# Kernel optimization log

Hardware: AMD Instinct MI355X
Metric: run time of the kernel (lower is better)

The kernel has to match this reference:

```python
import jax, jax.numpy as jnp
import numpy as np

NUM_FEATURE = 50


def setup_inputs() -> dict:
    key = jax.random.key(0)
    k1, k2 = jax.random.split(key)
    query = jax.random.normal(k1, (512, NUM_FEATURE), dtype=jnp.float32)
    doc = jax.random.normal(k2, (512, 256, NUM_FEATURE), dtype=jnp.float32)
    # nn.Linear(150, 1, bias=False) with weight filled with 1
    W = jnp.ones((3 * NUM_FEATURE,), dtype=jnp.float32)
    return {"query": query, "doc": doc, "W": W}


def reference(query, doc, W):
    # Split the single 150-dim linear weight into the three trilinear parts:
    # score(x, y) = w1.sen_x + w2.q_y + w3.(sen_x * q_y)
    w1, w2, w3 = W[:NUM_FEATURE], W[NUM_FEATURE:2 * NUM_FEATURE], W[2 * NUM_FEATURE:]
    q_term = query @ w2                      # [Lq]
    qw3 = query * w3                         # [Lq, d]

    def per_sentence(sen):                   # sen: [Ls, d]
        sXY = (sen @ w1)[:, None] + q_term[None, :] + sen @ qw3.T   # [Ls, Lq]
        sD2Q = jax.nn.softmax(sXY, axis=0)   # softmax over sentence tokens
        sQ2D = jax.nn.softmax(sXY, axis=1)   # softmax over query tokens
        aD2Q = sD2Q @ query                  # [Ls, d]
        aQ2D = sD2Q @ (sQ2D.T @ sen)         # (sD2Q @ sQ2D.T) @ sen, cheaper order
        return jnp.concatenate([sen, aD2Q, sen * aD2Q, sen * aQ2D], axis=1)  # [Ls, 4d]

    return jax.vmap(per_sentence)(doc)       # [n_sen, Ls, 4d]
```

## Files before the change

### kernel.cpp

```cpp
#include <hip/hip_runtime.h>
#include <math.h>

typedef __bf16 bf16_t;
typedef bf16_t bf16x2 __attribute__((ext_vector_type(2)));
typedef bf16_t bf16x4 __attribute__((ext_vector_type(4)));
typedef bf16_t bf16x8 __attribute__((ext_vector_type(8)));
typedef float f32x4 __attribute__((ext_vector_type(4)));

#define MFMA16(a,b,c) __builtin_amdgcn_mfma_f32_16x16x32_bf16((a),(b),(c),0,0,0)

#define ND 256
#define NQ 512
#define NF 50
#define L2E 1.44269504f
#define SHIFT 64.0f

#define SENT_E 0
#define PD0_E  16896
#define PD1_E  35328
#define QW3_E  53760
#define QTT_E  62976
#define KL0_E  16896
#define KL1_E  27136
#define EA_B   74752
#define PART_B  144384
#define STATS_B 148480
#define LDS_BYTES 151808

#define ST_QTERM 0
#define ST_CI    512
#define ST_RINV  576

__launch_bounds__(1024, 4)
__global__ void ca9_kernel(const float* __restrict__ query,
                           const float* __restrict__ doc,
                           const float* __restrict__ W,
                           float* __restrict__ out)
{
    extern __shared__ char smem[];
    bf16_t* lb = (bf16_t*)smem;
    float* part  = (float*)(smem + PART_B);
    float* stats = (float*)(smem + STATS_B);

    const int tid = threadIdx.x;
    const int w = tid >> 6, l = tid & 63, ln = l & 15, lg = l >> 4;
    const int s = blockIdx.x;
    const float* sen_g = doc + (size_t)s * (ND * NF);

    auto stageQW3 = [&](int jt, int buf, int tbase, int tn) {
        const int j0 = jt * 64;
        bf16_t* dst = lb + QW3_E + buf * 4608;
        for (int e = tid - tbase; e < 1664; e += tn) {
            int jj = e / 26, c = e - jj * 26;
            if (c < 25) {
                float2 v = ((const float2*)query)[(j0 + jj) * 25 + c];
                bf16x2 p;
                p[0] = (bf16_t)(v.x * W[100 + 2 * c] * L2E);
                p[1] = (bf16_t)(v.y * W[100 + 2 * c + 1] * L2E);
                *(bf16x2*)&dst[jj * 72 + 2 * c] = p;
            } else {
                bf16x2 p;
                p[0] = (bf16_t)(stats[ST_QTERM + j0 + jj] * L2E);
                p[1] = (bf16_t)L2E;
                *(bf16x2*)&dst[jj * 72 + 50] = p;
            }
        }
    };
    auto stageQTT = [&](int jt, int buf, int tbase, int tn) {
        const int j0 = jt * 64;
        bf16_t* dst = lb + QTT_E + buf * 4608;
        for (int e = tid - tbase; e < 1600; e += tn) {
            int c = e >> 6, jj = e & 63;
            float2 v = ((const float2*)query)[(j0 + jj) * 25 + c];
            dst[(2 * c) * 72 + jj]     = (bf16_t)v.x;
            dst[(2 * c + 1) * 72 + jj] = (bf16_t)v.y;
        }
    };

    for (int e = tid; e < 924; e += 1024) {
        int f = 50 + e / 66, c4 = (e - (e / 66) * 66) * 4;
        *(bf16x4*)&lb[SENT_E + f * 264 + c4] = (bf16x4){(bf16_t)0.f,(bf16_t)0.f,(bf16_t)0.f,(bf16_t)0.f};
    }
    for (int e = tid; e < 768; e += 1024) {
        int i = e / 3, c4 = 52 + (e - (e / 3) * 3) * 4;
        *(bf16x4*)&lb[PD0_E + i * 72 + c4] = (bf16x4){(bf16_t)0.f,(bf16_t)0.f,(bf16_t)0.f,(bf16_t)0.f};
    }
    for (int e = tid; e < 384; e += 1024) {
        int b = e / 192, r = e - b * 192;
        int jj = r / 3, c4 = 52 + (r - (r / 3) * 3) * 4;
        *(bf16x4*)&lb[QW3_E + b * 4608 + jj * 72 + c4] = (bf16x4){(bf16_t)0.f,(bf16_t)0.f,(bf16_t)0.f,(bf16_t)0.f};
    }
    for (int e = tid; e < 504; e += 1024) {
        int b = e / 252, r = e - b * 252;
        int f = 50 + r / 18, c4 = (r - (r / 18) * 18) * 4;
        *(bf16x4*)&lb[QTT_E + b * 4608 + f * 72 + c4] = (bf16x4){(bf16_t)0.f,(bf16_t)0.f,(bf16_t)0.f,(bf16_t)0.f};
    }
    for (int e = tid; e < 256 * 25; e += 1024) {
        int i = e / 25, c = e - i * 25;
        float2 v = ((const float2*)sen_g)[i * 25 + c];
        bf16x2 p; p[0] = (bf16_t)v.x; p[1] = (bf16_t)v.y;
        *(bf16x2*)&lb[PD0_E + i * 72 + 2 * c] = p;
        lb[SENT_E + (2 * c) * 264 + i]     = p[0];
        lb[SENT_E + (2 * c + 1) * 264 + i] = p[1];
    }
    if (tid < NQ) {
        float acc = 0.f;
        #pragma unroll
        for (int c = 0; c < 25; ++c) {
            float2 v = ((const float2*)query)[tid * 25 + c];
            acc += v.x * W[NF + 2 * c] + v.y * W[NF + 2 * c + 1];
        }
        stats[ST_QTERM + tid] = acc;
    }
    if (tid < ND) {
        float acc = 0.f;
        #pragma unroll
        for (int f = 0; f < NF; ++f) acc += sen_g[tid * NF + f] * W[f];
        lb[PD0_E + tid * 72 + 50] = (bf16_t)1.0f;
        lb[PD0_E + tid * 72 + 51] = (bf16_t)acc;
    }
    __syncthreads();

    bf16x8 aS[2];
    #pragma unroll
    for (int ks = 0; ks < 2; ++ks)
        aS[ks] = *(bf16x8*)&lb[PD0_E + (w * 16 + ln) * 72 + lg * 8 + ks * 32];
    stageQW3(0, 0, 0, 1024);
    stageQTT(0, 0, 0, 1024);
    __syncthreads();

    f32x4 accD[4];
    f32x4 K[9];
    #pragma unroll
    for (int nf = 0; nf < 4; ++nf) accD[nf] = (f32x4){0.f, 0.f, 0.f, 0.f};
    #pragma unroll
    for (int d = 0; d < 9; ++d) K[d] = (f32x4){0.f, 0.f, 0.f, 0.f};
    float rpart[4] = {0.f, 0.f, 0.f, 0.f};

    auto consumeTile = [&](const bf16_t* pdp, const bf16_t* qtp) {
        bf16x8 aPs[2];
        #pragma unroll
        for (int ks = 0; ks < 2; ++ks) {
            bf16x8 raw = *(bf16x8*)&pdp[(w * 16 + ln) * 72 + lg * 8 + ks * 32];
            float4 c0 = *(const float4*)&stats[ST_CI + lg * 8 + ks * 32];
            float4 c1 = *(const float4*)&stats[ST_CI + lg * 8 + ks * 32 + 4];
            aPs[ks][0] = (bf16_t)((float)raw[0] * c0.x);
            aPs[ks][1] = (bf16_t)((float)raw[1] * c0.y);
            aPs[ks][2] = (bf16_t)((float)raw[2] * c0.z);
            aPs[ks][3] = (bf16_t)((float)raw[3] * c0.w);
            aPs[ks][4] = (bf16_t)((float)raw[4] * c1.x);
            aPs[ks][5] = (bf16_t)((float)raw[5] * c1.y);
            aPs[ks][6] = (bf16_t)((float)raw[6] * c1.z);
            aPs[ks][7] = (bf16_t)((float)raw[7] * c1.w);
        }
        #pragma unroll
        for (int ks = 0; ks < 2; ++ks)
            #pragma unroll
            for (int nf = 0; nf < 4; ++nf) {
                bf16x8 bq = *(bf16x8*)&qtp[(nf * 16 + ln) * 72 + lg * 8 + ks * 32];
                accD[nf] = MFMA16(aPs[ks], bq, accD[nf]);
            }
        #pragma unroll
        for (int d = 0; d < 9; ++d) {
            if (d < 8 || w < 8) {
                const int cb = (w + d) & 15;
                #pragma unroll
                for (int ks = 0; ks < 2; ++ks) {
                    bf16x8 bb = *(bf16x8*)&pdp[(cb * 16 + ln) * 72 + lg * 8 + ks * 32];
                    K[d] = MFMA16(aPs[ks], bb, K[d]);
                }
            }
        }
    };

    for (int jt = 0; jt < 8; ++jt) {
        if (jt > 0) {
            const int pb = (jt - 1) & 1;
            consumeTile(lb + (pb ? PD1_E : PD0_E), lb + QTT_E + pb * 4608);
        }

        const bf16_t* qb = lb + QW3_E + (jt & 1) * 4608;
        bf16_t* pd = lb + ((jt & 1) ? PD1_E : PD0_E);
        f32x4 acc[4];
        #pragma unroll
        for (int nf = 0; nf < 4; ++nf) acc[nf] = (f32x4){-SHIFT, -SHIFT, -SHIFT, -SHIFT};
        #pragma unroll
        for (int ks = 0; ks < 2; ++ks)
            #pragma unroll
            for (int nf = 0; nf < 4; ++nf) {
                bf16x8 b = *(bf16x8*)&qb[(nf * 16 + ln) * 72 + lg * 8 + ks * 32];
                acc[nf] = MFMA16(aS[ks], b, acc[nf]);
            }
        #pragma unroll
        for (int nf = 0; nf < 4; ++nf) {
            #pragma unroll
            for (int r = 0; r < 4; ++r) acc[nf][r] = exp2f(acc[nf][r]);
            float cp = (acc[nf][0] + acc[nf][1]) + (acc[nf][2] + acc[nf][3]);
            cp += __shfl_xor(cp, 16);
            cp += __shfl_xor(cp, 32);
            if (lg == 0) part[w * 64 + nf * 16 + ln] = cp;
            #pragma unroll
            for (int r = 0; r < 4; ++r) {
                rpart[r] += acc[nf][r];
                pd[(w * 16 + lg * 4 + r) * 72 + nf * 16 + ln] = (bf16_t)acc[nf][r];
            }
        }
        __syncthreads();

        if (w == 0) {
            float cs = 0.f;
            #pragma unroll
            for (int ww = 0; ww < 16; ++ww) cs += part[ww * 64 + l];
            stats[ST_CI + l] = 1.f / cs;
        } else if (jt < 7) {
            stageQW3(jt + 1, (jt + 1) & 1, 64, 960);
            stageQTT(jt + 1, (jt + 1) & 1, 64, 960);
        }
        __syncthreads();
    }
    consumeTile(lb + PD1_E, lb + QTT_E + 4608);

    #pragma unroll
    for (int r = 0; r < 4; ++r) {
        float v = rpart[r];
        v += __shfl_xor(v, 1);
        v += __shfl_xor(v, 2);
        v += __shfl_xor(v, 4);
        v += __shfl_xor(v, 8);
        if (ln == 0) stats[ST_RINV + w * 16 + lg * 4 + r] = 1.f / v;
    }
    __syncthreads();

    float* ea = (float*)(smem + EA_B);
    #pragma unroll
    for (int nf = 0; nf < 4; ++nf)
        #pragma unroll
        for (int r = 0; r < 4; ++r)
            ea[(w * 16 + lg * 4 + r) * 68 + nf * 16 + ln] = accD[nf][r];

    f32x4 accQ[4];
    #pragma unroll
    for (int nf = 0; nf < 4; ++nf) accQ[nf] = (f32x4){0.f, 0.f, 0.f, 0.f};
    #pragma unroll
    for (int kt = 0; kt < 8; ++kt) {
        bf16_t* kl = lb + ((kt & 1) ? KL1_E : KL0_E);
        #pragma unroll
        for (int d = 0; d < 9; ++d) {
            if (d < 8 || w < 8) {
                const int cb = (w + d) & 15;
                if ((cb >> 1) == kt) {
                    const int h = cb & 1;
                    const float riv = stats[ST_RINV + cb * 16 + ln];
                    #pragma unroll
                    for (int r = 0; r < 4; ++r)
                        kl[(w * 16 + lg * 4 + r) * 40 + h * 16 + ln] =
                            (bf16_t)(K[d][r] * riv);
                }
            }
        }
        if ((w >> 1) == kt) {
            const int h = w & 1;
            float4 rv = *(const float4*)&stats[ST_RINV + w * 16 + lg * 4];
            #pragma unroll
            for (int d = 1; d < 9; ++d) {
                if (d < 8 || w < 8) {
                    const int cb = (w + d) & 15;
                    bf16x4 pk;
                    pk[0] = (bf16_t)(K[d][0] * rv.x);
                    pk[1] = (bf16_t)(K[d][1] * rv.y);
                    pk[2] = (bf16_t)(K[d][2] * rv.z);
                    pk[3] = (bf16_t)(K[d][3] * rv.w);
                    *(bf16x4*)&kl[(cb * 16 + ln) * 40 + h * 16 + lg * 4] = pk;
                }
            }
        }
        __syncthreads();
        bf16x8 aK = *(bf16x8*)&kl[(w * 16 + ln) * 40 + lg * 8];
        #pragma unroll
        for (int nf = 0; nf < 4; ++nf) {
            bf16x8 b = *(bf16x8*)&lb[SENT_E + (nf * 16 + ln) * 264 + kt * 32 + lg * 8];
            accQ[nf] = MFMA16(aK, b, accQ[nf]);
        }
    }
    __syncthreads();

    float* eb = (float*)smem;
    #pragma unroll
    for (int nf = 0; nf < 4; ++nf)
        #pragma unroll
        for (int r = 0; r < 4; ++r)
            eb[(w * 16 + lg * 4 + r) * 68 + nf * 16 + ln] = accQ[nf][r];
    __syncthreads();
    const size_t ob0 = (size_t)s * (ND * 200);
    #pragma unroll
    for (int seg = 0; seg < 4; ++seg) {
        for (int v = tid; v < 6400; v += 1024) {
            int i = v / 25, c = v - (v / 25) * 25;
            int f = 2 * c;
            float2 o;
            if (seg == 0) {
                o = *(const float2*)&sen_g[i * 50 + f];
            } else if (seg == 1) {
                o.x = ea[i * 68 + f]; o.y = ea[i * 68 + f + 1];
            } else if (seg == 2) {
                float2 d = *(const float2*)&sen_g[i * 50 + f];
                o.x = d.x * ea[i * 68 + f]; o.y = d.y * ea[i * 68 + f + 1];
            } else {
                float2 d = *(const float2*)&sen_g[i * 50 + f];
                o.x = d.x * eb[i * 68 + f]; o.y = d.y * eb[i * 68 + f + 1];
            }
            *(float2*)&out[ob0 + (size_t)i * 200 + seg * 50 + f] = o;
        }
    }
}

extern "C" void kernel_launch(void* const* d_in, const int* in_sizes, int n_in,
                              void* d_out, int out_size, void* d_ws, size_t ws_size,
                              hipStream_t stream) {
    const float* query = (const float*)d_in[0];
    const float* doc   = (const float*)d_in[1];
    const float* W     = (const float*)d_in[2];
    float* out = (float*)d_out;
    (void)d_ws; (void)ws_size; (void)n_in; (void)in_sizes; (void)out_size;

    hipFuncSetAttribute((const void*)ca9_kernel,
                        hipFuncAttributeMaxDynamicSharedMemorySize,
                        LDS_BYTES);
    ca9_kernel<<<dim3(512), dim3(1024), LDS_BYTES, stream>>>(query, doc, W, out);
}
```

Before: 132.6 us.

## Double-buffer column partials, compute inverses per wave, drop one barrier per tile

The per-tile column-sum partials are now double-buffered. Every wave computes its own column-sum reciprocal and broadcasts it with lane shuffles, so wave 0 no longer reduces serially and a second __syncthreads per tile is gone. Staging of the next query tiles is spread across all threads at the start of each iteration rather than split between waves 1-15. The sentence-by-w1 dot product also switches to float2 loads. In exchange, each wave repeats the partial reduction and uses more LDS for the second partial buffer.

```diff
diff --git a/kernel.cpp b/kernel.cpp
--- a/kernel.cpp
+++ b/kernel.cpp
@@ -24,18 +24,17 @@
 #define KL1_E  27136
 #define EA_B   74752
 #define PART_B  144384
-#define STATS_B 148480
-#define LDS_BYTES 151808
+#define STATS_B 152576
+#define LDS_BYTES 155648
 
 #define ST_QTERM 0
-#define ST_CI    512
-#define ST_RINV  576
+#define ST_RINV  512
 
 __launch_bounds__(1024, 4)
-__global__ void ca9_kernel(const float* __restrict__ query,
-                           const float* __restrict__ doc,
-                           const float* __restrict__ W,
-                           float* __restrict__ out)
+__global__ void ca13_kernel(const float* __restrict__ query,
+                            const float* __restrict__ doc,
+                            const float* __restrict__ W,
+                            float* __restrict__ out)
 {
     extern __shared__ char smem[];
     bf16_t* lb = (bf16_t*)smem;
@@ -47,10 +46,10 @@
     const int s = blockIdx.x;
     const float* sen_g = doc + (size_t)s * (ND * NF);
 
-    auto stageQW3 = [&](int jt, int buf, int tbase, int tn) {
+    auto stageQW3 = [&](int jt, int buf) {
         const int j0 = jt * 64;
         bf16_t* dst = lb + QW3_E + buf * 4608;
-        for (int e = tid - tbase; e < 1664; e += tn) {
+        for (int e = tid; e < 1664; e += 1024) {
             int jj = e / 26, c = e - jj * 26;
             if (c < 25) {
                 float2 v = ((const float2*)query)[(j0 + jj) * 25 + c];
@@ -66,10 +65,10 @@
             }
         }
     };
-    auto stageQTT = [&](int jt, int buf, int tbase, int tn) {
+    auto stageQTT = [&](int jt, int buf) {
         const int j0 = jt * 64;
         bf16_t* dst = lb + QTT_E + buf * 4608;
-        for (int e = tid - tbase; e < 1600; e += tn) {
+        for (int e = tid; e < 1600; e += 1024) {
             int c = e >> 6, jj = e & 63;
             float2 v = ((const float2*)query)[(j0 + jj) * 25 + c];
             dst[(2 * c) * 72 + jj]     = (bf16_t)v.x;
@@ -115,7 +114,10 @@
     if (tid < ND) {
         float acc = 0.f;
         #pragma unroll
-        for (int f = 0; f < NF; ++f) acc += sen_g[tid * NF + f] * W[f];
+        for (int c = 0; c < 25; ++c) {
+            float2 v = ((const float2*)sen_g)[tid * 25 + c];
+            acc += v.x * W[2 * c] + v.y * W[2 * c + 1];
+        }
         lb[PD0_E + tid * 72 + 50] = (bf16_t)1.0f;
         lb[PD0_E + tid * 72 + 51] = (bf16_t)acc;
     }
@@ -125,8 +127,7 @@
     #pragma unroll
     for (int ks = 0; ks < 2; ++ks)
         aS[ks] = *(bf16x8*)&lb[PD0_E + (w * 16 + ln) * 72 + lg * 8 + ks * 32];
-    stageQW3(0, 0, 0, 1024);
-    stageQTT(0, 0, 0, 1024);
+    stageQW3(0, 0);
     __syncthreads();
 
     f32x4 accD[4];
@@ -137,21 +138,16 @@
     for (int d = 0; d < 9; ++d) K[d] = (f32x4){0.f, 0.f, 0.f, 0.f};
     float rpart[4] = {0.f, 0.f, 0.f, 0.f};
 
-    auto consumeTile = [&](const bf16_t* pdp, const bf16_t* qtp) {
+    auto consumeTile = [&](const bf16_t* pdp, const bf16_t* qtp, float civ) {
         bf16x8 aPs[2];
         #pragma unroll
         for (int ks = 0; ks < 2; ++ks) {
             bf16x8 raw = *(bf16x8*)&pdp[(w * 16 + ln) * 72 + lg * 8 + ks * 32];
-            float4 c0 = *(const float4*)&stats[ST_CI + lg * 8 + ks * 32];
-            float4 c1 = *(const float4*)&stats[ST_CI + lg * 8 + ks * 32 + 4];
-            aPs[ks][0] = (bf16_t)((float)raw[0] * c0.x);
-            aPs[ks][1] = (bf16_t)((float)raw[1] * c0.y);
-            aPs[ks][2] = (bf16_t)((float)raw[2] * c0.z);
-            aPs[ks][3] = (bf16_t)((float)raw[3] * c0.w);
-            aPs[ks][4] = (bf16_t)((float)raw[4] * c1.x);
-            aPs[ks][5] = (bf16_t)((float)raw[5] * c1.y);
-            aPs[ks][6] = (bf16_t)((float)raw[6] * c1.z);
-            aPs[ks][7] = (bf16_t)((float)raw[7] * c1.w);
+            #pragma unroll
+            for (int e = 0; e < 8; ++e) {
+                float c = __shfl(civ, lg * 8 + ks * 32 + e);
+                aPs[ks][e] = (bf16_t)((float)raw[e] * c);
+            }
         }
         #pragma unroll
         for (int ks = 0; ks < 2; ++ks)
@@ -172,53 +168,52 @@
             }
         }
     };
+    auto colInv = [&](int pb) -> float {
+        const float* pp = part + pb * 1024;
+        float cs = 0.f;
+        #pragma unroll
+        for (int ww = 0; ww < 16; ++ww) cs += pp[ww * 64 + l];
+        return 1.f / cs;
+    };
 
     for (int jt = 0; jt < 8; ++jt) {
+        stageQTT(jt, jt & 1);
+        if (jt < 7) stageQW3(jt + 1, (jt + 1) & 1);
+
         if (jt > 0) {
             const int pb = (jt - 1) & 1;
-            consumeTile(lb + (pb ? PD1_E : PD0_E), lb + QTT_E + pb * 4608);
+            consumeTile(lb + (pb ? PD1_E : PD0_E), lb + QTT_E + pb * 4608, colInv(pb));
         }
 
         const bf16_t* qb = lb + QW3_E + (jt & 1) * 4608;
         bf16_t* pd = lb + ((jt & 1) ? PD1_E : PD0_E);
-        f32x4 acc[4];
-        #pragma unroll
-        for (int nf = 0; nf < 4; ++nf) acc[nf] = (f32x4){-SHIFT, -SHIFT, -SHIFT, -SHIFT};
+        f32x4 sacc[4];
+        #pragma unroll
+        for (int nf = 0; nf < 4; ++nf) sacc[nf] = (f32x4){-SHIFT, -SHIFT, -SHIFT, -SHIFT};
         #pragma unroll
         for (int ks = 0; ks < 2; ++ks)
             #pragma unroll
             for (int nf = 0; nf < 4; ++nf) {
                 bf16x8 b = *(bf16x8*)&qb[(nf * 16 + ln) * 72 + lg * 8 + ks * 32];
-                acc[nf] = MFMA16(aS[ks], b, acc[nf]);
+                sacc[nf] = MFMA16(aS[ks], b, sacc[nf]);
             }
         #pragma unroll
         for (int nf = 0; nf < 4; ++nf) {
             #pragma unroll
-            for (int r = 0; r < 4; ++r) acc[nf][r] = exp2f(acc[nf][r]);
-            float cp = (acc[nf][0] + acc[nf][1]) + (acc[nf][2] + acc[nf][3]);
+            for (int r = 0; r < 4; ++r) sacc[nf][r] = exp2f(sacc[nf][r]);
+            float cp = (sacc[nf][0] + sacc[nf][1]) + (sacc[nf][2] + sacc[nf][3]);
             cp += __shfl_xor(cp, 16);
             cp += __shfl_xor(cp, 32);
-            if (lg == 0) part[w * 64 + nf * 16 + ln] = cp;
+            if (lg == 0) part[(jt & 1) * 1024 + w * 64 + nf * 16 + ln] = cp;
             #pragma unroll
             for (int r = 0; r < 4; ++r) {
-                rpart[r] += acc[nf][r];
-                pd[(w * 16 + lg * 4 + r) * 72 + nf * 16 + ln] = (bf16_t)acc[nf][r];
+                rpart[r] += sacc[nf][r];
+                pd[(w * 16 + lg * 4 + r) * 72 + nf * 16 + ln] = (bf16_t)sacc[nf][r];
             }
         }
         __syncthreads();
-
-        if (w == 0) {
-            float cs = 0.f;
-            #pragma unroll
-            for (int ww = 0; ww < 16; ++ww) cs += part[ww * 64 + l];
-            stats[ST_CI + l] = 1.f / cs;
-        } else if (jt < 7) {
-            stageQW3(jt + 1, (jt + 1) & 1, 64, 960);
-            stageQTT(jt + 1, (jt + 1) & 1, 64, 960);
-        }
-        __syncthreads();
-    }
-    consumeTile(lb + PD1_E, lb + QTT_E + 4608);
+    }
+    consumeTile(lb + PD1_E, lb + QTT_E + 4608, colInv(1));
 
     #pragma unroll
     for (int r = 0; r < 4; ++r) {
@@ -323,8 +318,8 @@
     float* out = (float*)d_out;
     (void)d_ws; (void)ws_size; (void)n_in; (void)in_sizes; (void)out_size;
 
-    hipFuncSetAttribute((const void*)ca9_kernel,
+    hipFuncSetAttribute((const void*)ca13_kernel,
                         hipFuncAttributeMaxDynamicSharedMemorySize,
                         LDS_BYTES);
-    ca9_kernel<<<dim3(512), dim3(1024), LDS_BYTES, stream>>>(query, doc, W, out);
+    ca13_kernel<<<dim3(512), dim3(1024), LDS_BYTES, stream>>>(query, doc, W, out);
 }
```

Measured after the change: 151.3 us. 1.14x slower.
